# Performance work log

Measured on AMD Instinct MI355X. Metric: run time of the kernel, lower is better.

Reference implementation:

```python
import jax, jax.numpy as jnp
import numpy as np

BS, C, H, W, KSZ, NH = 4, 64, 64, 64, 7, 8
CH = 8 * C  # positional FFN hidden width (channels*8)


def _extract_nbhd(x, k):
    """x: (bs,h,w,d) -> (bs, h*w, k*k, d). Zero-padded k x k neighborhoods
    (the torch module unfolds the *projected* features, so padding zeros are
    zero keys/values, exactly as here)."""
    bs, h, w, d = x.shape
    p = k - 1
    xp = jnp.pad(x, ((0, 0), (p // 2, p - p // 2), (p // 2, p - p // 2), (0, 0)))
    shifts = [xp[:, di:di + h, dj:dj + w, :] for di in range(k) for dj in range(k)]
    patches = jnp.stack(shifts, axis=3)  # (bs, h, w, r, d)
    return patches.reshape(bs, h * w, k * k, d)


def setup_inputs() -> dict:
    key = jax.random.key(0)
    ks = jax.random.split(key, 8)

    def lin_w(kk, fan_in, fan_out):
        s = 1.0 / np.sqrt(fan_in)
        return jax.random.uniform(kk, (fan_in, fan_out), jnp.float32, -s, s)

    return {
        "x": jax.random.normal(ks[0], (BS, C, H, W), jnp.float32),
        "WQ_w": lin_w(ks[1], C, C), "WQ_b": jnp.zeros((C,), jnp.float32),
        "WK_w": lin_w(ks[2], C, C), "WK_b": jnp.zeros((C,), jnp.float32),
        "WV_w": lin_w(ks[3], C, C), "WV_b": jnp.zeros((C,), jnp.float32),
        "WO_w": lin_w(ks[4], C, C), "WO_b": jnp.zeros((C,), jnp.float32),
        "pos_w1": lin_w(ks[5], 2, CH), "pos_b1": jnp.zeros((CH,), jnp.float32),
        "pos_w2": lin_w(ks[6], CH, NH), "pos_b2": jnp.zeros((NH,), jnp.float32),
    }


def reference(x, WQ_w, WQ_b, WK_w, WK_b, WV_w, WV_b, WO_w, WO_b,
              pos_w1, pos_b1, pos_w2, pos_b2):
    bs, c, h, w = x.shape
    n, r, nh = h * w, KSZ * KSZ, NH
    dh = c // nh

    # ---- positional bias: FFN on relative coordinates of each k x k window ----
    gi, gj = jnp.meshgrid(jnp.linspace(-3.0, 3.0, h), jnp.linspace(-3.0, 3.0, w),
                          indexing='ij')
    coords = jnp.stack([gi, gj], axis=-1)                 # (h, w, 2)
    nb_coords = _extract_nbhd(coords[None], KSZ)          # (1, n, r, 2)
    rel = nb_coords - coords.reshape(1, n, 1, 2)          # (1, n, r, 2)
    P = jax.nn.relu(rel @ pos_w1 + pos_b1) @ pos_w2 + pos_b2   # (1, n, r, nh)

    # ---- restricted multi-head self attention over k x k neighborhoods ----
    xi = x.transpose(0, 2, 3, 1)                          # (bs, h, w, c)
    Q = (xi.reshape(bs, n, c) @ WQ_w + WQ_b).reshape(bs, n, nh, dh)
    Kn = _extract_nbhd(xi @ WK_w + WK_b, KSZ).reshape(bs, n, r, nh, dh)
    Vn = _extract_nbhd(xi @ WV_w + WV_b, KSZ).reshape(bs, n, r, nh, dh)

    scores = jnp.einsum('bnhd,bnrhd->bnhr', Q, Kn) / np.sqrt(dh).astype(np.float32)
    scores = scores + P.transpose(0, 1, 3, 2)             # bias per head, broadcast bs
    wts = jax.nn.softmax(scores, axis=-1)                 # (bs, n, nh, r)
    o = jnp.einsum('bnhr,bnrhd->bnhd', wts, Vn).reshape(bs, n, c)
    o = o @ WO_w + WO_b
    return o.reshape(bs, h, w, c).transpose(0, 3, 1, 2)   # (bs, c, h, w)
```

## Files before the change

### kernel.cpp

```cpp
#include <hip/hip_runtime.h>
#include <hip/hip_bf16.h>
#include <math.h>

#define NPIX   4096
#define STEPF  (6.0f/63.0f)
#define SCALE  0.35355339059327373f

#define OFF_PT 0
#define OFF_PB 4096
#define OFF_Q  65536
#define OFF_K  (OFF_Q + 1048576)
#define OFF_V  (OFF_K + 1048576)

__global__ __launch_bounds__(256) void pos_ffn_kernel(
    const float* __restrict__ w1, const float* __restrict__ b1,
    const float* __restrict__ w2, const float* __restrict__ b2,
    float* __restrict__ PT, float* __restrict__ PB)
{
    __shared__ float s_w1[1024];
    __shared__ float s_b1[512];
    __shared__ float s_w2[4096];
    int tid = threadIdx.x;
    for (int idx = tid; idx < 5632; idx += 256) {
        if (idx < 1024)       s_w1[idx]        = w1[idx];
        else if (idx < 1536)  s_b1[idx - 1024] = b1[idx - 1024];
        else                  s_w2[idx - 1536] = w2[idx - 1536];
    }
    __syncthreads();

    int gid = blockIdx.x * 256 + tid;
    int e  = gid >> 3;
    int lg = gid & 7;
    if (e >= 49 + NPIX) return;

    float r0, r1;
    if (e < 49) {
        int di = e / 7, dj = e % 7;
        r0 = (float)(di - 3) * STEPF;
        r1 = (float)(dj - 3) * STEPF;
    } else {
        int p = e - 49;
        r0 = 3.0f - (float)(p >> 6) * STEPF;
        r1 = 3.0f - (float)(p & 63) * STEPF;
    }

    float acc[8] = {0.f,0.f,0.f,0.f,0.f,0.f,0.f,0.f};
    #pragma unroll 8
    for (int kk = 0; kk < 64; ++kk) {
        int k = (kk << 3) + lg;
        float hv = fmaf(r0, s_w1[k], fmaf(r1, s_w1[512 + k], s_b1[k]));
        hv = fmaxf(hv, 0.0f);
        const float4 wa = *(const float4*)&s_w2[k * 8];
        const float4 wb = *(const float4*)&s_w2[k * 8 + 4];
        acc[0] = fmaf(hv, wa.x, acc[0]);
        acc[1] = fmaf(hv, wa.y, acc[1]);
        acc[2] = fmaf(hv, wa.z, acc[2]);
        acc[3] = fmaf(hv, wa.w, acc[3]);
        acc[4] = fmaf(hv, wb.x, acc[4]);
        acc[5] = fmaf(hv, wb.y, acc[5]);
        acc[6] = fmaf(hv, wb.z, acc[6]);
        acc[7] = fmaf(hv, wb.w, acc[7]);
    }
    #pragma unroll
    for (int m = 1; m < 8; m <<= 1) {
        #pragma unroll
        for (int j = 0; j < 8; ++j) acc[j] += __shfl_xor(acc[j], m);
    }
    float v = acc[lg] + b2[lg];
    if (e < 49) PT[e * 8 + lg] = v;
    else        PB[(e - 49) * 8 + lg] = v;
}

__global__ __launch_bounds__(256) void qkv_kernel(
    const float* __restrict__ x,
    const float* __restrict__ wq, const float* __restrict__ bq,
    const float* __restrict__ wk, const float* __restrict__ bk,
    const float* __restrict__ wv, const float* __restrict__ bv,
    float* __restrict__ Qo, float* __restrict__ Ko, float* __restrict__ Vo)
{
    __shared__ float s_W[4096];
    __shared__ float s_b[64];
    const float* W; const float* bias; float* out;
    if (blockIdx.y == 0)      { W = wq; bias = bq; out = Qo; }
    else if (blockIdx.y == 1) { W = wk; bias = bk; out = Ko; }
    else                      { W = wv; bias = bv; out = Vo; }

    int tid = threadIdx.x;
    {
        const float4* W4 = (const float4*)W;
        float4* s4 = (float4*)s_W;
        #pragma unroll
        for (int q = 0; q < 4; ++q) s4[tid + q * 256] = W4[tid + q * 256];
    }
    if (tid < 64) s_b[tid] = bias[tid];
    __syncthreads();

    int jg = tid & 3;
    int pl = tid >> 2;
    int g0 = blockIdx.x * 128;
    int b  = g0 >> 12;
    int p0 = g0 & 4095;
    const float* xb = x + ((size_t)b << 18) + p0 + pl;

    float accA[16], accB[16];
    #pragma unroll
    for (int jj = 0; jj < 16; ++jj) {
        float bv_ = s_b[(jg << 4) + jj];
        accA[jj] = bv_; accB[jj] = bv_;
    }

    #pragma unroll 4
    for (int c = 0; c < 64; ++c) {
        float xa = xb[(size_t)c << 12];
        float xc = xb[((size_t)c << 12) + 64];
        const float* wr = &s_W[(c << 6) + (jg << 4)];
        const float4 w0 = *(const float4*)(wr + 0);
        const float4 w1v = *(const float4*)(wr + 4);
        const float4 w2v = *(const float4*)(wr + 8);
        const float4 w3v = *(const float4*)(wr + 12);
        accA[0]  = fmaf(xa, w0.x,  accA[0]);  accB[0]  = fmaf(xc, w0.x,  accB[0]);
        accA[1]  = fmaf(xa, w0.y,  accA[1]);  accB[1]  = fmaf(xc, w0.y,  accB[1]);
        accA[2]  = fmaf(xa, w0.z,  accA[2]);  accB[2]  = fmaf(xc, w0.z,  accB[2]);
        accA[3]  = fmaf(xa, w0.w,  accA[3]);  accB[3]  = fmaf(xc, w0.w,  accB[3]);
        accA[4]  = fmaf(xa, w1v.x, accA[4]);  accB[4]  = fmaf(xc, w1v.x, accB[4]);
        accA[5]  = fmaf(xa, w1v.y, accA[5]);  accB[5]  = fmaf(xc, w1v.y, accB[5]);
        accA[6]  = fmaf(xa, w1v.z, accA[6]);  accB[6]  = fmaf(xc, w1v.z, accB[6]);
        accA[7]  = fmaf(xa, w1v.w, accA[7]);  accB[7]  = fmaf(xc, w1v.w, accB[7]);
        accA[8]  = fmaf(xa, w2v.x, accA[8]);  accB[8]  = fmaf(xc, w2v.x, accB[8]);
        accA[9]  = fmaf(xa, w2v.y, accA[9]);  accB[9]  = fmaf(xc, w2v.y, accB[9]);
        accA[10] = fmaf(xa, w2v.z, accA[10]); accB[10] = fmaf(xc, w2v.z, accB[10]);
        accA[11] = fmaf(xa, w2v.w, accA[11]); accB[11] = fmaf(xc, w2v.w, accB[11]);
        accA[12] = fmaf(xa, w3v.x, accA[12]); accB[12] = fmaf(xc, w3v.x, accB[12]);
        accA[13] = fmaf(xa, w3v.y, accA[13]); accB[13] = fmaf(xc, w3v.y, accB[13]);
        accA[14] = fmaf(xa, w3v.z, accA[14]); accB[14] = fmaf(xc, w3v.z, accB[14]);
        accA[15] = fmaf(xa, w3v.w, accA[15]); accB[15] = fmaf(xc, w3v.w, accB[15]);
    }

    float* opA = out + (size_t)(g0 + pl) * 64 + (jg << 4);
    float* opB = opA + 64 * 64;
    *(float4*)(opA + 0)  = make_float4(accA[0],  accA[1],  accA[2],  accA[3]);
    *(float4*)(opA + 4)  = make_float4(accA[4],  accA[5],  accA[6],  accA[7]);
    *(float4*)(opA + 8)  = make_float4(accA[8],  accA[9],  accA[10], accA[11]);
    *(float4*)(opA + 12) = make_float4(accA[12], accA[13], accA[14], accA[15]);
    *(float4*)(opB + 0)  = make_float4(accB[0],  accB[1],  accB[2],  accB[3]);
    *(float4*)(opB + 4)  = make_float4(accB[4],  accB[5],  accB[6],  accB[7]);
    *(float4*)(opB + 8)  = make_float4(accB[8],  accB[9],  accB[10], accB[11]);
    *(float4*)(opB + 12) = make_float4(accB[12], accB[13], accB[14], accB[15]);
}

__global__ __launch_bounds__(256) void attn_fused_kernel(
    const float* __restrict__ Q, const float* __restrict__ K,
    const float* __restrict__ V, const float* __restrict__ PT,
    const float* __restrict__ PB, const float* __restrict__ WO,
    const float* __restrict__ bO, float* __restrict__ out)
{
    __shared__ float s_PT[392];
    __shared__ float s_W[4096];
    __shared__ float s_b[64];
    __shared__ float s_O[32 * 68];
    int tid = threadIdx.x;
    {
        const float4* W4 = (const float4*)WO;
        float4* s4 = (float4*)s_W;
        #pragma unroll
        for (int q = 0; q < 4; ++q) s4[tid + q * 256] = W4[tid + q * 256];
    }
    for (int idx = tid; idx < 392; idx += 256) s_PT[idx] = PT[idx];
    if (tid < 64) s_b[tid] = bO[tid];
    __syncthreads();

    int t = blockIdx.x * 256 + tid;
    int h = t & 7;
    int p = (t >> 3) & 4095;
    int b = t >> 15;
    int i = p >> 6, j = p & 63;

    const float* qp = Q + ((size_t)((b << 12) + p) << 6) + (h << 3);
    const float4 qa = *(const float4*)qp;
    const float4 qb = *(const float4*)(qp + 4);
    const float* Kbh = K + ((size_t)b << 18) + (h << 3);
    const float* Vbh = V + ((size_t)b << 18) + (h << 3);
    const float pb = PB[(p << 3) + h];

    float sc[49];
    float mx = -1e30f;
    #pragma unroll
    for (int di = 0; di < 7; ++di) {
        int i2 = i + di - 3;
        bool iok = (unsigned)i2 < 64u;
        int i2c = i2 < 0 ? 0 : (i2 > 63 ? 63 : i2);
        #pragma unroll
        for (int dj = 0; dj < 7; ++dj) {
            int j2 = j + dj - 3;
            bool ok = iok && ((unsigned)j2 < 64u);
            int j2c = j2 < 0 ? 0 : (j2 > 63 ? 63 : j2);
            const float* kp = Kbh + (i2c << 12) + (j2c << 6);
            const float4 ka = *(const float4*)kp;
            const float4 kb = *(const float4*)(kp + 4);
            float da = fmaf(qa.y, ka.y, qa.x * ka.x);
            da = fmaf(qa.w, ka.w, fmaf(qa.z, ka.z, da));
            float db = fmaf(qb.y, kb.y, qb.x * kb.x);
            db = fmaf(qb.w, kb.w, fmaf(qb.z, kb.z, db));
            int r = di * 7 + dj;
            float s = fmaf(da + db, SCALE, s_PT[(r << 3) + h]);
            s = ok ? s : pb;
            sc[r] = s;
            mx = fmaxf(mx, s);
        }
    }

    float sum = 0.0f;
    float o0=0.f,o1=0.f,o2=0.f,o3=0.f,o4=0.f,o5=0.f,o6=0.f,o7=0.f;
    #pragma unroll
    for (int di = 0; di < 7; ++di) {
        int i2 = i + di - 3;
        bool iok = (unsigned)i2 < 64u;
        int i2c = i2 < 0 ? 0 : (i2 > 63 ? 63 : i2);
        #pragma unroll
        for (int dj = 0; dj < 7; ++dj) {
            int j2 = j + dj - 3;
            bool ok = iok && ((unsigned)j2 < 64u);
            int j2c = j2 < 0 ? 0 : (j2 > 63 ? 63 : j2);
            int r = di * 7 + dj;
            float e = __expf(sc[r] - mx);
            sum += e;
            float ew = ok ? e : 0.0f;
            const float* vp = Vbh + (i2c << 12) + (j2c << 6);
            const float4 va = *(const float4*)vp;
            const float4 vb = *(const float4*)(vp + 4);
            o0 = fmaf(ew, va.x, o0); o1 = fmaf(ew, va.y, o1);
            o2 = fmaf(ew, va.z, o2); o3 = fmaf(ew, va.w, o3);
            o4 = fmaf(ew, vb.x, o4); o5 = fmaf(ew, vb.y, o5);
            o6 = fmaf(ew, vb.z, o6); o7 = fmaf(ew, vb.w, o7);
        }
    }
    float inv = 1.0f / sum;
    {
        int pl = (tid >> 3) & 31;
        float* so = &s_O[pl * 68 + (h << 3)];
        *(float4*)(so + 0) = make_float4(o0 * inv, o1 * inv, o2 * inv, o3 * inv);
        *(float4*)(so + 4) = make_float4(o4 * inv, o5 * inv, o6 * inv, o7 * inv);
    }
    __syncthreads();

    int pl2 = tid & 31;
    int cg  = tid >> 5;
    float acc[8];
    #pragma unroll
    for (int k = 0; k < 8; ++k) acc[k] = s_b[(cg << 3) + k];

    #pragma unroll 8
    for (int c = 0; c < 64; ++c) {
        float xv = s_O[pl2 * 68 + c];
        const float* wr = &s_W[(c << 6) + (cg << 3)];
        const float4 wa = *(const float4*)wr;
        const float4 wb = *(const float4*)(wr + 4);
        acc[0] = fmaf(xv, wa.x, acc[0]); acc[1] = fmaf(xv, wa.y, acc[1]);
        acc[2] = fmaf(xv, wa.z, acc[2]); acc[3] = fmaf(xv, wa.w, acc[3]);
        acc[4] = fmaf(xv, wb.x, acc[4]); acc[5] = fmaf(xv, wb.y, acc[5]);
        acc[6] = fmaf(xv, wb.z, acc[6]); acc[7] = fmaf(xv, wb.w, acc[7]);
    }

    int g0 = blockIdx.x * 32;
    int bb = g0 >> 12;
    int pp = (g0 & 4095) + pl2;
    float* ob = out + ((size_t)bb << 18) + pp;
    #pragma unroll
    for (int k = 0; k < 8; ++k) ob[(size_t)((cg << 3) + k) << 12] = acc[k];
}

extern "C" void kernel_launch(void* const* d_in, const int* in_sizes, int n_in,
                              void* d_out, int out_size, void* d_ws, size_t ws_size,
                              hipStream_t stream) {
    const float* x    = (const float*)d_in[0];
    const float* WQw  = (const float*)d_in[1];
    const float* WQb  = (const float*)d_in[2];
    const float* WKw  = (const float*)d_in[3];
    const float* WKb  = (const float*)d_in[4];
    const float* WVw  = (const float*)d_in[5];
    const float* WVb  = (const float*)d_in[6];
    const float* WOw  = (const float*)d_in[7];
    const float* WOb  = (const float*)d_in[8];
    const float* pw1  = (const float*)d_in[9];
    const float* pb1  = (const float*)d_in[10];
    const float* pw2  = (const float*)d_in[11];
    const float* pb2  = (const float*)d_in[12];

    float* ws = (float*)d_ws;
    float* PT = ws + OFF_PT;
    float* PB = ws + OFF_PB;
    float* Qb = ws + OFF_Q;
    float* Kb = ws + OFF_K;
    float* Vb = ws + OFF_V;

    pos_ffn_kernel<<<((49 + NPIX) * 8 + 255) / 256, 256, 0, stream>>>(
        pw1, pb1, pw2, pb2, PT, PB);
    qkv_kernel<<<dim3(16384 / 128, 3), 256, 0, stream>>>(
        x, WQw, WQb, WKw, WKb, WVw, WVb, Qb, Kb, Vb);
    attn_fused_kernel<<<131072 / 256, 256, 0, stream>>>(
        Qb, Kb, Vb, PT, PB, WOw, WOb, (float*)d_out);
}
```

Baseline: 55.21 us.

## Merge positional FFN into QKV kernel and stage K/V halos in shared memory

The positional-FFN and QKV projection kernels are merged into one launch, with blocks dispatched by index, which removes one kernel launch. The QKV part now computes four pixels per thread using float4 x loads. The attention kernel maps each block to a 32-pixel row segment and cooperatively loads the 7x38 K and then V halo tiles into shared memory, replacing per-thread scattered global loads. The same shared buffer is reused for WO, and PT is kept in registers. The cost is more LDS use, extra barriers and higher register pressure.

```diff
diff --git a/kernel.cpp b/kernel.cpp
--- a/kernel.cpp
+++ b/kernel.cpp
@@ -12,175 +12,197 @@
 #define OFF_K  (OFF_Q + 1048576)
 #define OFF_V  (OFF_K + 1048576)
 
-__global__ __launch_bounds__(256) void pos_ffn_kernel(
-    const float* __restrict__ w1, const float* __restrict__ b1,
-    const float* __restrict__ w2, const float* __restrict__ b2,
-    float* __restrict__ PT, float* __restrict__ PB)
-{
-    __shared__ float s_w1[1024];
-    __shared__ float s_b1[512];
-    __shared__ float s_w2[4096];
-    int tid = threadIdx.x;
-    for (int idx = tid; idx < 5632; idx += 256) {
-        if (idx < 1024)       s_w1[idx]        = w1[idx];
-        else if (idx < 1536)  s_b1[idx - 1024] = b1[idx - 1024];
-        else                  s_w2[idx - 1536] = w2[idx - 1536];
-    }
-    __syncthreads();
-
-    int gid = blockIdx.x * 256 + tid;
-    int e  = gid >> 3;
-    int lg = gid & 7;
-    if (e >= 49 + NPIX) return;
-
-    float r0, r1;
-    if (e < 49) {
-        int di = e / 7, dj = e % 7;
-        r0 = (float)(di - 3) * STEPF;
-        r1 = (float)(dj - 3) * STEPF;
-    } else {
-        int p = e - 49;
-        r0 = 3.0f - (float)(p >> 6) * STEPF;
-        r1 = 3.0f - (float)(p & 63) * STEPF;
-    }
-
-    float acc[8] = {0.f,0.f,0.f,0.f,0.f,0.f,0.f,0.f};
-    #pragma unroll 8
-    for (int kk = 0; kk < 64; ++kk) {
-        int k = (kk << 3) + lg;
-        float hv = fmaf(r0, s_w1[k], fmaf(r1, s_w1[512 + k], s_b1[k]));
-        hv = fmaxf(hv, 0.0f);
-        const float4 wa = *(const float4*)&s_w2[k * 8];
-        const float4 wb = *(const float4*)&s_w2[k * 8 + 4];
-        acc[0] = fmaf(hv, wa.x, acc[0]);
-        acc[1] = fmaf(hv, wa.y, acc[1]);
-        acc[2] = fmaf(hv, wa.z, acc[2]);
-        acc[3] = fmaf(hv, wa.w, acc[3]);
-        acc[4] = fmaf(hv, wb.x, acc[4]);
-        acc[5] = fmaf(hv, wb.y, acc[5]);
-        acc[6] = fmaf(hv, wb.z, acc[6]);
-        acc[7] = fmaf(hv, wb.w, acc[7]);
-    }
-    #pragma unroll
-    for (int m = 1; m < 8; m <<= 1) {
-        #pragma unroll
-        for (int j = 0; j < 8; ++j) acc[j] += __shfl_xor(acc[j], m);
-    }
-    float v = acc[lg] + b2[lg];
-    if (e < 49) PT[e * 8 + lg] = v;
-    else        PB[(e - 49) * 8 + lg] = v;
-}
-
-__global__ __launch_bounds__(256) void qkv_kernel(
+__global__ __launch_bounds__(256, 2) void pos_qkv_kernel(
     const float* __restrict__ x,
     const float* __restrict__ wq, const float* __restrict__ bq,
     const float* __restrict__ wk, const float* __restrict__ bk,
     const float* __restrict__ wv, const float* __restrict__ bv,
-    float* __restrict__ Qo, float* __restrict__ Ko, float* __restrict__ Vo)
+    const float* __restrict__ pw1, const float* __restrict__ pb1,
+    const float* __restrict__ pw2, const float* __restrict__ pb2,
+    float* __restrict__ Qo, float* __restrict__ Ko, float* __restrict__ Vo,
+    float* __restrict__ PT, float* __restrict__ PB)
 {
-    __shared__ float s_W[4096];
-    __shared__ float s_b[64];
-    const float* W; const float* bias; float* out;
-    if (blockIdx.y == 0)      { W = wq; bias = bq; out = Qo; }
-    else if (blockIdx.y == 1) { W = wk; bias = bk; out = Ko; }
-    else                      { W = wv; bias = bv; out = Vo; }
-
+    __shared__ __align__(16) float smem[5632];
     int tid = threadIdx.x;
-    {
-        const float4* W4 = (const float4*)W;
-        float4* s4 = (float4*)s_W;
-        #pragma unroll
-        for (int q = 0; q < 4; ++q) s4[tid + q * 256] = W4[tid + q * 256];
-    }
-    if (tid < 64) s_b[tid] = bias[tid];
-    __syncthreads();
-
-    int jg = tid & 3;
-    int pl = tid >> 2;
-    int g0 = blockIdx.x * 128;
-    int b  = g0 >> 12;
-    int p0 = g0 & 4095;
-    const float* xb = x + ((size_t)b << 18) + p0 + pl;
-
-    float accA[16], accB[16];
-    #pragma unroll
-    for (int jj = 0; jj < 16; ++jj) {
-        float bv_ = s_b[(jg << 4) + jj];
-        accA[jj] = bv_; accB[jj] = bv_;
-    }
-
-    #pragma unroll 4
-    for (int c = 0; c < 64; ++c) {
-        float xa = xb[(size_t)c << 12];
-        float xc = xb[((size_t)c << 12) + 64];
-        const float* wr = &s_W[(c << 6) + (jg << 4)];
-        const float4 w0 = *(const float4*)(wr + 0);
-        const float4 w1v = *(const float4*)(wr + 4);
-        const float4 w2v = *(const float4*)(wr + 8);
-        const float4 w3v = *(const float4*)(wr + 12);
-        accA[0]  = fmaf(xa, w0.x,  accA[0]);  accB[0]  = fmaf(xc, w0.x,  accB[0]);
-        accA[1]  = fmaf(xa, w0.y,  accA[1]);  accB[1]  = fmaf(xc, w0.y,  accB[1]);
-        accA[2]  = fmaf(xa, w0.z,  accA[2]);  accB[2]  = fmaf(xc, w0.z,  accB[2]);
-        accA[3]  = fmaf(xa, w0.w,  accA[3]);  accB[3]  = fmaf(xc, w0.w,  accB[3]);
-        accA[4]  = fmaf(xa, w1v.x, accA[4]);  accB[4]  = fmaf(xc, w1v.x, accB[4]);
-        accA[5]  = fmaf(xa, w1v.y, accA[5]);  accB[5]  = fmaf(xc, w1v.y, accB[5]);
-        accA[6]  = fmaf(xa, w1v.z, accA[6]);  accB[6]  = fmaf(xc, w1v.z, accB[6]);
-        accA[7]  = fmaf(xa, w1v.w, accA[7]);  accB[7]  = fmaf(xc, w1v.w, accB[7]);
-        accA[8]  = fmaf(xa, w2v.x, accA[8]);  accB[8]  = fmaf(xc, w2v.x, accB[8]);
-        accA[9]  = fmaf(xa, w2v.y, accA[9]);  accB[9]  = fmaf(xc, w2v.y, accB[9]);
-        accA[10] = fmaf(xa, w2v.z, accA[10]); accB[10] = fmaf(xc, w2v.z, accB[10]);
-        accA[11] = fmaf(xa, w2v.w, accA[11]); accB[11] = fmaf(xc, w2v.w, accB[11]);
-        accA[12] = fmaf(xa, w3v.x, accA[12]); accB[12] = fmaf(xc, w3v.x, accB[12]);
-        accA[13] = fmaf(xa, w3v.y, accA[13]); accB[13] = fmaf(xc, w3v.y, accB[13]);
-        accA[14] = fmaf(xa, w3v.z, accA[14]); accB[14] = fmaf(xc, w3v.z, accB[14]);
-        accA[15] = fmaf(xa, w3v.w, accA[15]); accB[15] = fmaf(xc, w3v.w, accB[15]);
-    }
-
-    float* opA = out + (size_t)(g0 + pl) * 64 + (jg << 4);
-    float* opB = opA + 64 * 64;
-    *(float4*)(opA + 0)  = make_float4(accA[0],  accA[1],  accA[2],  accA[3]);
-    *(float4*)(opA + 4)  = make_float4(accA[4],  accA[5],  accA[6],  accA[7]);
-    *(float4*)(opA + 8)  = make_float4(accA[8],  accA[9],  accA[10], accA[11]);
-    *(float4*)(opA + 12) = make_float4(accA[12], accA[13], accA[14], accA[15]);
-    *(float4*)(opB + 0)  = make_float4(accB[0],  accB[1],  accB[2],  accB[3]);
-    *(float4*)(opB + 4)  = make_float4(accB[4],  accB[5],  accB[6],  accB[7]);
-    *(float4*)(opB + 8)  = make_float4(accB[8],  accB[9],  accB[10], accB[11]);
-    *(float4*)(opB + 12) = make_float4(accB[12], accB[13], accB[14], accB[15]);
+    int bid = blockIdx.x;
+
+    if (bid < 192) {
+        int mat = bid >> 6;
+        const float* W; const float* bias; float* out;
+        if (mat == 0)      { W = wq; bias = bq; out = Qo; }
+        else if (mat == 1) { W = wk; bias = bk; out = Ko; }
+        else               { W = wv; bias = bv; out = Vo; }
+
+        float* s_W = smem;
+        float* s_b = smem + 4096;
+        {
+            const float4* W4 = (const float4*)W;
+            float4* s4 = (float4*)s_W;
+            #pragma unroll
+            for (int q = 0; q < 4; ++q) s4[tid + q * 256] = W4[tid + q * 256];
+        }
+        if (tid < 64) s_b[tid] = bias[tid];
+        __syncthreads();
+
+        int jg = tid & 3;
+        int pl = tid >> 2;
+        int pxblk = bid & 63;
+        int g0 = pxblk << 8;
+        int b  = g0 >> 12;
+        int pp = g0 & 4095;
+        const float* xb = x + ((size_t)b << 18) + pp + (pl << 2);
+
+        float acc[4][16];
+        #pragma unroll
+        for (int jj = 0; jj < 16; ++jj) {
+            float bv_ = s_b[(jg << 4) + jj];
+            acc[0][jj] = bv_; acc[1][jj] = bv_; acc[2][jj] = bv_; acc[3][jj] = bv_;
+        }
+
+        #pragma unroll 2
+        for (int c = 0; c < 64; ++c) {
+            float4 xv = *(const float4*)(xb + ((size_t)c << 12));
+            const float* wr = &s_W[(c << 6) + (jg << 4)];
+            const float4 w0 = *(const float4*)(wr + 0);
+            const float4 w1v = *(const float4*)(wr + 4);
+            const float4 w2v = *(const float4*)(wr + 8);
+            const float4 w3v = *(const float4*)(wr + 12);
+            float xs[4] = {xv.x, xv.y, xv.z, xv.w};
+            #pragma unroll
+            for (int e = 0; e < 4; ++e) {
+                float xe = xs[e];
+                acc[e][0]  = fmaf(xe, w0.x,  acc[e][0]);
+                acc[e][1]  = fmaf(xe, w0.y,  acc[e][1]);
+                acc[e][2]  = fmaf(xe, w0.z,  acc[e][2]);
+                acc[e][3]  = fmaf(xe, w0.w,  acc[e][3]);
+                acc[e][4]  = fmaf(xe, w1v.x, acc[e][4]);
+                acc[e][5]  = fmaf(xe, w1v.y, acc[e][5]);
+                acc[e][6]  = fmaf(xe, w1v.z, acc[e][6]);
+                acc[e][7]  = fmaf(xe, w1v.w, acc[e][7]);
+                acc[e][8]  = fmaf(xe, w2v.x, acc[e][8]);
+                acc[e][9]  = fmaf(xe, w2v.y, acc[e][9]);
+                acc[e][10] = fmaf(xe, w2v.z, acc[e][10]);
+                acc[e][11] = fmaf(xe, w2v.w, acc[e][11]);
+                acc[e][12] = fmaf(xe, w3v.x, acc[e][12]);
+                acc[e][13] = fmaf(xe, w3v.y, acc[e][13]);
+                acc[e][14] = fmaf(xe, w3v.z, acc[e][14]);
+                acc[e][15] = fmaf(xe, w3v.w, acc[e][15]);
+            }
+        }
+
+        #pragma unroll
+        for (int e = 0; e < 4; ++e) {
+            float* op = out + (size_t)(g0 + (pl << 2) + e) * 64 + (jg << 4);
+            *(float4*)(op + 0)  = make_float4(acc[e][0],  acc[e][1],  acc[e][2],  acc[e][3]);
+            *(float4*)(op + 4)  = make_float4(acc[e][4],  acc[e][5],  acc[e][6],  acc[e][7]);
+            *(float4*)(op + 8)  = make_float4(acc[e][8],  acc[e][9],  acc[e][10], acc[e][11]);
+            *(float4*)(op + 12) = make_float4(acc[e][12], acc[e][13], acc[e][14], acc[e][15]);
+        }
+    } else {
+        float* s_w1 = smem;
+        float* s_b1 = smem + 1024;
+        float* s_w2 = smem + 1536;
+        {
+            float4* s4 = (float4*)smem;
+            s4[tid] = ((const float4*)pw1)[tid];
+            if (tid < 128) ((float4*)s_b1)[tid] = ((const float4*)pb1)[tid];
+            float4* w24 = (float4*)s_w2;
+            #pragma unroll
+            for (int q = 0; q < 4; ++q) w24[tid + q * 256] = ((const float4*)pw2)[tid + q * 256];
+        }
+        __syncthreads();
+
+        int base = (bid - 192) << 5;
+        int e  = base + (tid >> 3);
+        int lg = tid & 7;
+        if (e >= 49 + NPIX) return;
+
+        float r0, r1;
+        if (e < 49) {
+            int di = e / 7, dj = e % 7;
+            r0 = (float)(di - 3) * STEPF;
+            r1 = (float)(dj - 3) * STEPF;
+        } else {
+            int pq = e - 49;
+            r0 = 3.0f - (float)(pq >> 6) * STEPF;
+            r1 = 3.0f - (float)(pq & 63) * STEPF;
+        }
+
+        float acc[8] = {0.f,0.f,0.f,0.f,0.f,0.f,0.f,0.f};
+        #pragma unroll 8
+        for (int kk = 0; kk < 64; ++kk) {
+            int k = (kk << 3) + lg;
+            float hv = fmaf(r0, s_w1[k], fmaf(r1, s_w1[512 + k], s_b1[k]));
+            hv = fmaxf(hv, 0.0f);
+            const float4 wa = *(const float4*)&s_w2[k * 8];
+            const float4 wb = *(const float4*)&s_w2[k * 8 + 4];
+            acc[0] = fmaf(hv, wa.x, acc[0]);
+            acc[1] = fmaf(hv, wa.y, acc[1]);
+            acc[2] = fmaf(hv, wa.z, acc[2]);
+            acc[3] = fmaf(hv, wa.w, acc[3]);
+            acc[4] = fmaf(hv, wb.x, acc[4]);
+            acc[5] = fmaf(hv, wb.y, acc[5]);
+            acc[6] = fmaf(hv, wb.z, acc[6]);
+            acc[7] = fmaf(hv, wb.w, acc[7]);
+        }
+        #pragma unroll
+        for (int m = 1; m < 8; m <<= 1) {
+            #pragma unroll
+            for (int jx = 0; jx < 8; ++jx) acc[jx] += __shfl_xor(acc[jx], m);
+        }
+        float v = acc[lg] + pb2[lg];
+        if (e < 49) PT[e * 8 + lg] = v;
+        else        PB[(e - 49) * 8 + lg] = v;
+    }
 }
 
-__global__ __launch_bounds__(256) void attn_fused_kernel(
+__global__ __launch_bounds__(256, 2) void attn_fused_kernel(
     const float* __restrict__ Q, const float* __restrict__ K,
     const float* __restrict__ V, const float* __restrict__ PT,
     const float* __restrict__ PB, const float* __restrict__ WO,
     const float* __restrict__ bO, float* __restrict__ out)
 {
-    __shared__ float s_PT[392];
-    __shared__ float s_W[4096];
-    __shared__ float s_b[64];
-    __shared__ float s_O[32 * 68];
-    int tid = threadIdx.x;
-    {
-        const float4* W4 = (const float4*)WO;
-        float4* s4 = (float4*)s_W;
-        #pragma unroll
-        for (int q = 0; q < 4; ++q) s4[tid + q * 256] = W4[tid + q * 256];
-    }
-    for (int idx = tid; idx < 392; idx += 256) s_PT[idx] = PT[idx];
-    if (tid < 64) s_b[tid] = bO[tid];
-    __syncthreads();
-
-    int t = blockIdx.x * 256 + tid;
-    int h = t & 7;
-    int p = (t >> 3) & 4095;
-    int b = t >> 15;
-    int i = p >> 6, j = p & 63;
+    __shared__ __align__(16) float s_KV[7 * 38 * 68];
+    __shared__ __align__(16) float s_O[32 * 68];
+    __shared__ float s_bias[64];
+
+    int tid  = threadIdx.x;
+    int bid  = blockIdx.x;
+    int b    = bid >> 7;
+    int pblk = bid & 127;
+    int i    = pblk >> 1;
+    int j0   = (pblk & 1) << 5;
+    int h    = tid & 7;
+    int pxl  = tid >> 3;
+    int j    = j0 + pxl;
+    int p    = (i << 6) + j;
+
+    if (tid < 64) s_bias[tid] = bO[tid];
+
+    float pt[49];
+    #pragma unroll
+    for (int r = 0; r < 49; ++r) pt[r] = PT[(r << 3) + h];
+    float pbv = PB[(p << 3) + h];
 
     const float* qp = Q + ((size_t)((b << 12) + p) << 6) + (h << 3);
     const float4 qa = *(const float4*)qp;
     const float4 qb = *(const float4*)(qp + 4);
-    const float* Kbh = K + ((size_t)b << 18) + (h << 3);
-    const float* Vbh = V + ((size_t)b << 18) + (h << 3);
-    const float pb = PB[(p << 3) + h];
+
+    const float* Kb = K + ((size_t)b << 18);
+    const float* Vb = V + ((size_t)b << 18);
+
+    #pragma unroll
+    for (int r = 0; r < 7; ++r) {
+        int ic = i - 3 + r; ic = ic < 0 ? 0 : (ic > 63 ? 63 : ic);
+        const float* rowb = Kb + ((size_t)ic << 12);
+        for (int v = tid; v < 608; v += 256) {
+            int cc = v >> 4, q4 = v & 15;
+            int jc = j0 - 3 + cc; jc = jc < 0 ? 0 : (jc > 63 ? 63 : jc);
+            *(float4*)&s_KV[(r * 38 + cc) * 68 + (q4 << 2)] =
+                *(const float4*)(rowb + (jc << 6) + (q4 << 2));
+        }
+    }
+    __syncthreads();
 
     float sc[49];
     float mx = -1e30f;
@@ -188,26 +210,39 @@
     for (int di = 0; di < 7; ++di) {
         int i2 = i + di - 3;
         bool iok = (unsigned)i2 < 64u;
-        int i2c = i2 < 0 ? 0 : (i2 > 63 ? 63 : i2);
+        const float* krow = &s_KV[(di * 38 + pxl) * 68 + (h << 3)];
         #pragma unroll
         for (int dj = 0; dj < 7; ++dj) {
             int j2 = j + dj - 3;
             bool ok = iok && ((unsigned)j2 < 64u);
-            int j2c = j2 < 0 ? 0 : (j2 > 63 ? 63 : j2);
-            const float* kp = Kbh + (i2c << 12) + (j2c << 6);
-            const float4 ka = *(const float4*)kp;
-            const float4 kb = *(const float4*)(kp + 4);
+            const float* kp = krow + dj * 68;
+            const float4 ka  = *(const float4*)kp;
+            const float4 kb2 = *(const float4*)(kp + 4);
             float da = fmaf(qa.y, ka.y, qa.x * ka.x);
             da = fmaf(qa.w, ka.w, fmaf(qa.z, ka.z, da));
-            float db = fmaf(qb.y, kb.y, qb.x * kb.x);
-            db = fmaf(qb.w, kb.w, fmaf(qb.z, kb.z, db));
+            float db = fmaf(qb.y, kb2.y, qb.x * kb2.x);
+            db = fmaf(qb.w, kb2.w, fmaf(qb.z, kb2.z, db));
             int r = di * 7 + dj;
-            float s = fmaf(da + db, SCALE, s_PT[(r << 3) + h]);
-            s = ok ? s : pb;
+            float s = fmaf(da + db, SCALE, pt[r]);
+            s = ok ? s : pbv;
             sc[r] = s;
             mx = fmaxf(mx, s);
         }
     }
+    __syncthreads();
+
+    #pragma unroll
+    for (int r = 0; r < 7; ++r) {
+        int ic = i - 3 + r; ic = ic < 0 ? 0 : (ic > 63 ? 63 : ic);
+        const float* rowb = Vb + ((size_t)ic << 12);
+        for (int v = tid; v < 608; v += 256) {
+            int cc = v >> 4, q4 = v & 15;
+            int jc = j0 - 3 + cc; jc = jc < 0 ? 0 : (jc > 63 ? 63 : jc);
+            *(float4*)&s_KV[(r * 38 + cc) * 68 + (q4 << 2)] =
+                *(const float4*)(rowb + (jc << 6) + (q4 << 2));
+        }
+    }
+    __syncthreads();
 
     float sum = 0.0f;
     float o0=0.f,o1=0.f,o2=0.f,o3=0.f,o4=0.f,o5=0.f,o6=0.f,o7=0.f;
@@ -215,31 +250,37 @@
     for (int di = 0; di < 7; ++di) {
         int i2 = i + di - 3;
         bool iok = (unsigned)i2 < 64u;
-        int i2c = i2 < 0 ? 0 : (i2 > 63 ? 63 : i2);
+        const float* vrow = &s_KV[(di * 38 + pxl) * 68 + (h << 3)];
         #pragma unroll
         for (int dj = 0; dj < 7; ++dj) {
             int j2 = j + dj - 3;
             bool ok = iok && ((unsigned)j2 < 64u);
-            int j2c = j2 < 0 ? 0 : (j2 > 63 ? 63 : j2);
             int r = di * 7 + dj;
             float e = __expf(sc[r] - mx);
             sum += e;
             float ew = ok ? e : 0.0f;
-            const float* vp = Vbh + (i2c << 12) + (j2c << 6);
-            const float4 va = *(const float4*)vp;
-            const float4 vb = *(const float4*)(vp + 4);
+            const float* vp = vrow + dj * 68;
+            const float4 va  = *(const float4*)vp;
+            const float4 vb2 = *(const float4*)(vp + 4);
             o0 = fmaf(ew, va.x, o0); o1 = fmaf(ew, va.y, o1);
             o2 = fmaf(ew, va.z, o2); o3 = fmaf(ew, va.w, o3);
-            o4 = fmaf(ew, vb.x, o4); o5 = fmaf(ew, vb.y, o5);
-            o6 = fmaf(ew, vb.z, o6); o7 = fmaf(ew, vb.w, o7);
+            o4 = fmaf(ew, vb2.x, o4); o5 = fmaf(ew, vb2.y, o5);
+            o6 = fmaf(ew, vb2.z, o6); o7 = fmaf(ew, vb2.w, o7);
         }
     }
     float inv = 1.0f / sum;
     {
-        int pl = (tid >> 3) & 31;
-        float* so = &s_O[pl * 68 + (h << 3)];
+        float* so = &s_O[pxl * 68 + (h << 3)];
         *(float4*)(so + 0) = make_float4(o0 * inv, o1 * inv, o2 * inv, o3 * inv);
         *(float4*)(so + 4) = make_float4(o4 * inv, o5 * inv, o6 * inv, o7 * inv);
+    }
+    __syncthreads();
+
+    {
+        const float4* W4 = (const float4*)WO;
+        float4* d4 = (float4*)s_KV;
+        #pragma unroll
+        for (int q = 0; q < 4; ++q) d4[tid + q * 256] = W4[tid + q * 256];
     }
     __syncthreads();
 
@@ -247,24 +288,28 @@
     int cg  = tid >> 5;
     float acc[8];
     #pragma unroll
-    for (int k = 0; k < 8; ++k) acc[k] = s_b[(cg << 3) + k];
-
-    #pragma unroll 8
-    for (int c = 0; c < 64; ++c) {
-        float xv = s_O[pl2 * 68 + c];
-        const float* wr = &s_W[(c << 6) + (cg << 3)];
-        const float4 wa = *(const float4*)wr;
-        const float4 wb = *(const float4*)(wr + 4);
-        acc[0] = fmaf(xv, wa.x, acc[0]); acc[1] = fmaf(xv, wa.y, acc[1]);
-        acc[2] = fmaf(xv, wa.z, acc[2]); acc[3] = fmaf(xv, wa.w, acc[3]);
-        acc[4] = fmaf(xv, wb.x, acc[4]); acc[5] = fmaf(xv, wb.y, acc[5]);
-        acc[6] = fmaf(xv, wb.z, acc[6]); acc[7] = fmaf(xv, wb.w, acc[7]);
-    }
-
-    int g0 = blockIdx.x * 32;
-    int bb = g0 >> 12;
-    int pp = (g0 & 4095) + pl2;
-    float* ob = out + ((size_t)bb << 18) + pp;
+    for (int k = 0; k < 8; ++k) acc[k] = s_bias[(cg << 3) + k];
+
+    #pragma unroll 4
+    for (int c4 = 0; c4 < 16; ++c4) {
+        float4 xv = *(const float4*)&s_O[pl2 * 68 + (c4 << 2)];
+        float xs[4] = {xv.x, xv.y, xv.z, xv.w};
+        #pragma unroll
+        for (int e = 0; e < 4; ++e) {
+            int c = (c4 << 2) + e;
+            const float* wr = &s_KV[(c << 6) + (cg << 3)];
+            const float4 wa = *(const float4*)wr;
+            const float4 wb = *(const float4*)(wr + 4);
+            float xe = xs[e];
+            acc[0] = fmaf(xe, wa.x, acc[0]); acc[1] = fmaf(xe, wa.y, acc[1]);
+            acc[2] = fmaf(xe, wa.z, acc[2]); acc[3] = fmaf(xe, wa.w, acc[3]);
+            acc[4] = fmaf(xe, wb.x, acc[4]); acc[5] = fmaf(xe, wb.y, acc[5]);
+            acc[6] = fmaf(xe, wb.z, acc[6]); acc[7] = fmaf(xe, wb.w, acc[7]);
+        }
+    }
+
+    int p0 = (i << 6) + j0;
+    float* ob = out + ((size_t)b << 18) + p0 + pl2;
     #pragma unroll
     for (int k = 0; k < 8; ++k) ob[(size_t)((cg << 3) + k) << 12] = acc[k];
 }
@@ -293,10 +338,9 @@
     float* Kb = ws + OFF_K;
     float* Vb = ws + OFF_V;
 
-    pos_ffn_kernel<<<((49 + NPIX) * 8 + 255) / 256, 256, 0, stream>>>(
-        pw1, pb1, pw2, pb2, PT, PB);
-    qkv_kernel<<<dim3(16384 / 128, 3), 256, 0, stream>>>(
-        x, WQw, WQb, WKw, WKb, WVw, WVb, Qb, Kb, Vb);
-    attn_fused_kernel<<<131072 / 256, 256, 0, stream>>>(
+    pos_qkv_kernel<<<322, 256, 0, stream>>>(
+        x, WQw, WQb, WKw, WKb, WVw, WVb, pw1, pb1, pw2, pb2,
+        Qb, Kb, Vb, PT, PB);
+    attn_fused_kernel<<<512, 256, 0, stream>>>(
         Qb, Kb, Vb, PT, PB, WOw, WOb, (float*)d_out);
 }
```

New measurement: 54.06 us. -2.1%, faster.
